# Optimization experiments

Measured on AMD Instinct MI355X. Metric: run time of the kernel, lower is better.

The kernel has to match this reference:

```python
import jax, jax.numpy as jnp
import numpy as np

B, H, W = 16, 16, 16
DIM = 768
NH = 8
HD = DIM // NH
NEXP = 8
TOPK = 2
DSTATE = 1
DTRANK = 4
KDIR = 4


def setup_inputs() -> dict:
    key = jax.random.key(0)
    ks = jax.random.split(key, 16)
    s = 1.0 / float(np.sqrt(DIM))
    inp = {
        'x': jax.random.normal(ks[0], (B, H, W, DIM)),
        'sa_in_w': jax.random.normal(ks[1], (3 * DIM, DIM)) * s,
        'sa_in_b': jnp.zeros((3 * DIM,)),
        'sa_out_w': jax.random.normal(ks[2], (DIM, DIM)) * s,
        'sa_out_b': jnp.zeros((DIM,)),
        'ca_in_w': jax.random.normal(ks[3], (2 * DIM, DIM)) * s,
        'ca_in_b': jnp.zeros((2 * DIM,)),
        'expert_queries': jax.random.normal(ks[4], (NEXP, DIM)) * s,
        'e_in_w': jax.random.normal(ks[5], (NEXP, 2 * DIM, DIM)) * s,
        'e_in_b': jnp.zeros((NEXP, 2 * DIM)),
        'e_conv_w': jax.random.normal(ks[6], (NEXP, DIM, 1, 3, 3)) / 3.0,
        'e_conv_b': jnp.zeros((NEXP, DIM)),
        'e_xproj_w': jax.random.normal(ks[7], (NEXP, KDIR, DTRANK + 2 * DSTATE, DIM)) * s,
        'e_dtproj_w': jax.random.normal(ks[8], (NEXP, KDIR, DIM, DTRANK)) * 0.1,
        'e_dtproj_b': jax.random.uniform(ks[9], (NEXP, KDIR, DIM), minval=-4.0, maxval=-2.0),
        'e_Alog': jax.random.uniform(ks[10], (NEXP, KDIR, DIM, DSTATE), minval=0.0, maxval=1.0),
        'e_D': jnp.ones((NEXP, KDIR, DIM)),
        'e_ln_scale': jnp.ones((NEXP, DIM)),
        'e_ln_bias': jnp.zeros((NEXP, DIM)),
    }
    return {k: v.astype(jnp.float32) for k, v in inp.items()}


def _selective_scan(xs, Wx, Wdt, bdt, Alog, D):
    # xs: [B, L, d]; Wx: [R+2N, d]; Wdt: [d, R]; Alog: [d, N]; D: [d]
    dbl = jnp.einsum('bld,ed->ble', xs, Wx)
    dt = jax.nn.softplus(jnp.einsum('blr,dr->bld', dbl[..., :DTRANK], Wdt) + bdt)
    Bm = dbl[..., DTRANK:DTRANK + DSTATE]
    Cm = dbl[..., DTRANK + DSTATE:]
    A = -jnp.exp(Alog)  # [d, N]

    def step(h, t):
        dt_t, B_t, C_t, x_t = t  # [b,d],[b,N],[b,N],[b,d]
        h = jnp.exp(dt_t[:, :, None] * A) * h + (dt_t * x_t)[:, :, None] * B_t[:, None, :]
        return h, jnp.einsum('bdn,bn->bd', h, C_t)

    b, L, d = xs.shape
    h0 = jnp.zeros((b, d, DSTATE), xs.dtype)
    tm = lambda a: jnp.moveaxis(a, 1, 0)
    _, ys = jax.lax.scan(step, h0, (tm(dt), tm(Bm), tm(Cm), tm(xs)))
    return jnp.moveaxis(ys, 0, 1) + D * xs


def _expert(in_w, in_b, conv_w, conv_b, xproj_w, dtp_w, dtp_b, Alog, D, ln_s, ln_b, x):
    b = x.shape[0]
    xz = jnp.einsum('bhwc,oc->bhwo', x, in_w) + in_b
    xc, z = jnp.split(xz, 2, axis=-1)
    xn = jax.lax.conv_general_dilated(jnp.transpose(xc, (0, 3, 1, 2)), conv_w,
                                      (1, 1), ((1, 1), (1, 1)), feature_group_count=DIM)
    xc = jax.nn.silu(jnp.transpose(xn + conv_b[None, :, None, None], (0, 2, 3, 1)))
    L = H * W
    xh = xc.reshape(b, L, DIM)                              # row-major 'h'
    xv = jnp.transpose(xc, (0, 2, 1, 3)).reshape(b, L, DIM)  # col-major 'v'
    seqs = jnp.stack([xh, xh[:, ::-1], xv, xv[:, ::-1]])     # [4, b, L, d]
    ys = jax.vmap(_selective_scan)(seqs, xproj_w, dtp_w, dtp_b, Alog, D)
    yv = ys[2] + ys[3][:, ::-1]
    yv = jnp.transpose(yv.reshape(b, W, H, DIM), (0, 2, 1, 3)).reshape(b, L, DIM)
    y = (ys[0] + ys[1][:, ::-1] + yv).reshape(b, H, W, DIM)
    mu = y.mean(-1, keepdims=True)
    var = ((y - mu) ** 2).mean(-1, keepdims=True)
    y = (y - mu) * jax.lax.rsqrt(var + 1e-5) * ln_s + ln_b   # out_norm (LayerNorm)
    y = y * jax.nn.silu(z)
    return y.mean((1, 2))  # AdaptiveAvgPool2d((1,1)) -> [b, DIM]


def _forward(x, sa_in_w, sa_in_b, sa_out_w, sa_out_b, ca_in_w, ca_in_b, expert_queries,
             e_in_w, e_in_b, e_conv_w, e_conv_b, e_xproj_w, e_dtproj_w, e_dtproj_b,
             e_Alog, e_D, e_ln_scale, e_ln_bias):
    b = x.shape[0]
    L = H * W
    scale = 1.0 / float(np.sqrt(HD))
    xs = x.reshape(b, L, DIM)
    # spatial self-attention (eval mode: dropout off)
    qkv = xs @ sa_in_w.T + sa_in_b
    q, k, v = [a.reshape(b, L, NH, HD) for a in jnp.split(qkv, 3, -1)]
    att = jax.nn.softmax(jnp.einsum('bqhd,bkhd->bhqk', q, k) * scale, -1)
    ctx = jnp.einsum('bhqk,bkhd->bqhd', att, v).reshape(b, L, DIM) @ sa_out_w.T + sa_out_b
    # expert cross-attention: only head-averaged attention weights are used
    q2 = (ctx @ ca_in_w[:DIM].T + ca_in_b[:DIM]).reshape(b, L, NH, HD)
    k2 = (expert_queries @ ca_in_w[DIM:].T + ca_in_b[DIM:]).reshape(NEXP, NH, HD)
    aw = jax.nn.softmax(jnp.einsum('blhd,ehd->bhle', q2, k2) * scale, -1).mean(1)  # [b,L,E]
    gate = jax.nn.softmax(aw.mean(1), -1)  # [b, E]
    tk_scores, tk_idx = jax.lax.top_k(gate, TOPK)
    wgt = jax.nn.softmax(tk_scores, -1)
    # dense expert compute (all experts on all samples), then gather top-k
    all_out = jax.vmap(_expert, in_axes=(0,) * 11 + (None,))(
        e_in_w, e_in_b, e_conv_w, e_conv_b, e_xproj_w, e_dtproj_w, e_dtproj_b,
        e_Alog, e_D, e_ln_scale, e_ln_bias, x)  # [E, b, DIM]
    per_b = jnp.transpose(all_out, (1, 0, 2))  # [b, E, DIM]
    sel = jnp.take_along_axis(per_b, tk_idx[:, :, None], axis=1)  # [b, K, DIM]
    return jnp.sum(wgt[:, :, None] * sel, axis=1)  # [b, DIM]


def reference(x, sa_in_w, sa_in_b, sa_out_w, sa_out_b, ca_in_w, ca_in_b, expert_queries,
              e_in_w, e_in_b, e_conv_w, e_conv_b, e_xproj_w, e_dtproj_w, e_dtproj_b,
              e_Alog, e_D, e_ln_scale, e_ln_bias):
    return _forward(x, sa_in_w, sa_in_b, sa_out_w, sa_out_b, ca_in_w, ca_in_b, expert_queries,
                    e_in_w, e_in_b, e_conv_w, e_conv_b, e_xproj_w, e_dtproj_w, e_dtproj_b,
                    e_Alog, e_D, e_ln_scale, e_ln_bias)
```

## Files before the change

### kernel.cpp

```cpp
#include <hip/hip_runtime.h>
#include <hip/hip_bf16.h>


#define LTOK 256
#define DIMC 768

typedef unsigned short ushortt;
typedef __attribute__((ext_vector_type(8))) short bf16x8;
typedef __attribute__((ext_vector_type(4))) float f32x4;

#define LOG2E 1.44269504f
#define LN2   0.69314718f

__device__ __forceinline__ float fexp2(float x) { return __builtin_amdgcn_exp2f(x); }
__device__ __forceinline__ float flog2(float x) { return __builtin_amdgcn_logf(x); }

__device__ __forceinline__ ushortt f2b(float f) {
  union { float f; unsigned u; } c; c.f = f;
  unsigned r = (c.u + 0x7FFFu + ((c.u >> 16) & 1u)) >> 16;
  return (ushortt)r;
}

__global__ __launch_bounds__(256) void mk_mcast4(
    const float* __restrict__ s0, ushortt* __restrict__ d0,
    const float* __restrict__ s1, ushortt* __restrict__ d1,
    const float* __restrict__ s2, ushortt* __restrict__ d2,
    const float* __restrict__ s3, ushortt* __restrict__ d3)
{
  long g = (long)blockIdx.x * 256 + threadIdx.x;
  const float* s; ushortt* dst; long o;
  if (g < 786432)       { s = s0; dst = d0; o = g; }
  else if (g < 1228800) { s = s1; dst = d1; o = g - 786432; }
  else if (g < 1376256) { s = s2; dst = d2; o = g - 1228800; }
  else                  { s = s3; dst = d3; o = g - 1376256; }
  o <<= 2;
  float4 v = *(const float4*)(s + o);
  ushort4 w;
  w.x = f2b(v.x); w.y = f2b(v.y); w.z = f2b(v.z); w.w = f2b(v.w);
  *(ushort4*)(dst + o) = w;
}

__global__ __launch_bounds__(256) void mk_cast(const float* __restrict__ in,
                                               ushortt* __restrict__ outp, long n)
{
  long i = ((long)blockIdx.x * 256 + threadIdx.x) * 4;
  if (i + 3 < n) {
    float4 v = *(const float4*)(in + i);
    ushort4 o;
    o.x = f2b(v.x); o.y = f2b(v.y); o.z = f2b(v.z); o.w = f2b(v.w);
    *(ushort4*)(outp + i) = o;
  }
}

__global__ __launch_bounds__(256) void mk_mfma(
    const ushortt* __restrict__ A, const ushortt* __restrict__ B,
    const float* __restrict__ bias, void* __restrict__ C,
    int K, int lda, int ldb, int ldc,
    long sA, long sB, long sC, long sBias,
    const int* __restrict__ pairExp, int tilesN,
    int outBf, int splitN, void* __restrict__ C2, int ldc2)
{
  int z = blockIdx.y;
  long aoff = 0, boff = 0, coff = 0, biasoff = 0;
  if (pairExp) {
    int e = pairExp[z];
    aoff = (long)(z >> 1) * sA; boff = (long)e * sB;
    coff = (long)z * sC; biasoff = (long)e * sBias;
  }
  int tile = blockIdx.x;
  int tm = tile / tilesN, tn = tile - tm * tilesN;
  long m0 = (long)tm << 7, n0 = (long)tn << 7;

  __shared__ ushortt As[128][40];
  __shared__ ushortt Bs[128][40];

  int tid = threadIdx.x;
  int lane = tid & 63, wvi = tid >> 6;
  int wr = wvi >> 1, wc = wvi & 1;
  int lm = lane & 15, lg = lane >> 4;

  f32x4 zero4 = {0.f, 0.f, 0.f, 0.f};
  f32x4 acc[4][4];
#pragma unroll
  for (int i = 0; i < 4; i++)
#pragma unroll
    for (int j = 0; j < 4; j++) acc[i][j] = zero4;

  const ushortt* Ab = A + aoff;
  const ushortt* Bb = B + boff;

  for (int k0 = 0; k0 < K; k0 += 32) {
#pragma unroll
    for (int h = 0; h < 2; h++) {
      int q = tid + h * 256;
      int row = q >> 2, ck = (q & 3) << 3;
      *(uint4*)&As[row][ck] = *(const uint4*)(Ab + (m0 + row) * lda + k0 + ck);
      *(uint4*)&Bs[row][ck] = *(const uint4*)(Bb + (n0 + row) * ldb + k0 + ck);
    }
    __syncthreads();
    bf16x8 af[4], bfr[4];
#pragma unroll
    for (int i = 0; i < 4; i++)
      af[i] = *(const bf16x8*)&As[wr * 64 + i * 16 + lm][lg << 3];
#pragma unroll
    for (int j = 0; j < 4; j++)
      bfr[j] = *(const bf16x8*)&Bs[wc * 64 + j * 16 + lm][lg << 3];
#pragma unroll
    for (int i = 0; i < 4; i++)
#pragma unroll
      for (int j = 0; j < 4; j++)
        acc[i][j] = __builtin_amdgcn_mfma_f32_16x16x32_bf16(af[i], bfr[j], acc[i][j], 0, 0, 0);
    __syncthreads();
  }

#pragma unroll
  for (int mt = 0; mt < 4; mt++) {
#pragma unroll
    for (int nt = 0; nt < 4; nt++) {
      long grow = m0 + wr * 64 + mt * 16 + lg * 4;
      long gcol = n0 + wc * 64 + nt * 16 + lm;
      float bv = bias ? bias[biasoff + gcol] : 0.f;
      void* Ct; long col; int ld;
      if ((int)gcol < splitN) { Ct = C; col = gcol; ld = ldc; }
      else { Ct = C2; col = gcol - splitN; ld = ldc2; }
#pragma unroll
      for (int r = 0; r < 4; r++) {
        float v = acc[mt][nt][r] + bv;
        long idx = coff + (grow + r) * ld + col;
        if (outBf) ((ushortt*)Ct)[idx] = f2b(v);
        else ((float*)Ct)[idx] = v;
      }
    }
  }
}

__global__ __launch_bounds__(256) void mk_gemm(
    const float* __restrict__ A, const float* __restrict__ B,
    const float* __restrict__ bias, void* __restrict__ C,
    int M, int N, int K, int lda, int ldb, int ldc,
    int zdiv,
    long sA1, long sA2, long sB1, long sB2, long sC1, long sC2,
    int bIsNT, int tilesN, int outBf)
{
  int z = blockIdx.y;
  int z1 = z / zdiv, z2 = z - z1 * zdiv;
  const float* Ab = A + (long)z1 * sA1 + (long)z2 * sA2;
  const float* Bb = B + (long)z1 * sB1 + (long)z2 * sB2;
  long coff = (long)z1 * sC1 + (long)z2 * sC2;

  int tile = blockIdx.x;
  int tm = tile / tilesN, tn = tile - tm * tilesN;
  int m0 = tm << 6, n0 = tn << 6;

  __shared__ float As[16][68];
  __shared__ float Bs[16][68];

  int tid = threadIdx.x;
  int tx = tid & 15, ty = tid >> 4;
  int lrow = tid >> 2;
  int lk = (tid & 3) << 2;
  int bkk = tid >> 4;
  int bnn = (tid & 15) << 2;

  float acc[4][4];
#pragma unroll
  for (int i = 0; i < 4; i++)
#pragma unroll
    for (int j = 0; j < 4; j++) acc[i][j] = 0.f;

  for (int k0 = 0; k0 < K; k0 += 16) {
    {
      int gm = m0 + lrow;
      float4 v = {0.f, 0.f, 0.f, 0.f};
      if (gm < M) v = *(const float4*)(Ab + (long)gm * lda + (k0 + lk));
      As[lk + 0][lrow] = v.x; As[lk + 1][lrow] = v.y;
      As[lk + 2][lrow] = v.z; As[lk + 3][lrow] = v.w;
    }
    if (bIsNT) {
      int gn = n0 + lrow;
      float4 v = {0.f, 0.f, 0.f, 0.f};
      if (gn < N) v = *(const float4*)(Bb + (long)gn * ldb + (k0 + lk));
      Bs[lk + 0][lrow] = v.x; Bs[lk + 1][lrow] = v.y;
      Bs[lk + 2][lrow] = v.z; Bs[lk + 3][lrow] = v.w;
    } else {
      int gn = n0 + bnn;
      float4 v = {0.f, 0.f, 0.f, 0.f};
      if (gn + 3 < N) {
        v = *(const float4*)(Bb + (long)(k0 + bkk) * ldb + gn);
      } else {
        float t0 = (gn + 0 < N) ? Bb[(long)(k0 + bkk) * ldb + gn + 0] : 0.f;
        float t1 = (gn + 1 < N) ? Bb[(long)(k0 + bkk) * ldb + gn + 1] : 0.f;
        float t2 = (gn + 2 < N) ? Bb[(long)(k0 + bkk) * ldb + gn + 2] : 0.f;
        float t3 = (gn + 3 < N) ? Bb[(long)(k0 + bkk) * ldb + gn + 3] : 0.f;
        v.x = t0; v.y = t1; v.z = t2; v.w = t3;
      }
      *(float4*)&Bs[bkk][bnn] = v;
    }
    __syncthreads();
#pragma unroll
    for (int kk = 0; kk < 16; kk++) {
      float4 a = *(const float4*)&As[kk][ty << 2];
      float4 b = *(const float4*)&Bs[kk][tx << 2];
      acc[0][0] += a.x * b.x; acc[0][1] += a.x * b.y; acc[0][2] += a.x * b.z; acc[0][3] += a.x * b.w;
      acc[1][0] += a.y * b.x; acc[1][1] += a.y * b.y; acc[1][2] += a.y * b.z; acc[1][3] += a.y * b.w;
      acc[2][0] += a.z * b.x; acc[2][1] += a.z * b.y; acc[2][2] += a.z * b.z; acc[2][3] += a.z * b.w;
      acc[3][0] += a.w * b.x; acc[3][1] += a.w * b.y; acc[3][2] += a.w * b.z; acc[3][3] += a.w * b.w;
    }
    __syncthreads();
  }

#pragma unroll
  for (int i = 0; i < 4; i++) {
    int gm = m0 + (ty << 2) + i;
    if (gm >= M) continue;
#pragma unroll
    for (int j = 0; j < 4; j++) {
      int gn = n0 + (tx << 2) + j;
      if (gn >= N) continue;
      float v = acc[i][j];
      if (bias) v += bias[gn];
      long idx = coff + (long)gm * ldc + gn;
      if (outBf) ((ushortt*)C)[idx] = f2b(v);
      else ((float*)C)[idx] = v;
    }
  }
}

__global__ __launch_bounds__(256) void mk_softmax(float* __restrict__ scores, float scale)
{
  int row = (blockIdx.x << 2) + (threadIdx.x >> 6);
  int lane = threadIdx.x & 63;
  float* p = scores + (long)row * 256 + (lane << 2);
  float4 v = *(const float4*)p;
  float m = fmaxf(fmaxf(v.x, v.y), fmaxf(v.z, v.w));
#pragma unroll
  for (int o = 32; o; o >>= 1) m = fmaxf(m, __shfl_xor(m, o, 64));
  float sl = scale * LOG2E;
  v.x = fexp2(sl * (v.x - m));
  v.y = fexp2(sl * (v.y - m));
  v.z = fexp2(sl * (v.z - m));
  v.w = fexp2(sl * (v.w - m));
  float s = v.x + v.y + v.z + v.w;
#pragma unroll
  for (int o = 32; o; o >>= 1) s += __shfl_xor(s, o, 64);
  float r = 1.f / s;
  v.x *= r; v.y *= r; v.z *= r; v.w *= r;
  *(float4*)p = v;
}

__global__ __launch_bounds__(256) void mk_gates(const float* __restrict__ q2,
                                                const float* __restrict__ k2,
                                                float* __restrict__ gacc)
{
  __shared__ float k2p[8 * 808];
  int b = blockIdx.x >> 4, q = blockIdx.x & 15;
  for (int i = threadIdx.x; i < 6144; i += 256) {
    int e = i / 768, rem = i - e * 768;
    int h = rem / 96, j = rem - h * 96;
    k2p[e * 808 + h * 100 + j] = k2[i];
  }
  __syncthreads();
  const float scale = 0.10206207261596577f;
  int wid = threadIdx.x >> 6, lane = threadIdx.x & 63;
  int h = lane >> 3, e = lane & 7;
  const float* kp = &k2p[e * 808 + h * 100];
  float accL = 0.f;
#pragma unroll
  for (int ti = 0; ti < 4; ti++) {
    int l = q * 16 + wid * 4 + ti;
    const float* qh = q2 + ((long)b * LTOK + l) * DIMC + h * 96;
    float sum = 0.f;
#pragma unroll
    for (int j = 0; j < 96; j += 4) {
      float4 qv = *(const float4*)(qh + j);
      float4 kv = *(const float4*)(kp + j);
      sum += qv.x * kv.x + qv.y * kv.y + qv.z * kv.z + qv.w * kv.w;
    }
    float s = sum * scale;
    float mx = s;
#pragma unroll
    for (int o = 1; o <= 4; o <<= 1) mx = fmaxf(mx, __shfl_xor(mx, o, 64));
    float ex = fexp2((s - mx) * LOG2E);
    float se = ex;
#pragma unroll
    for (int o = 1; o <= 4; o <<= 1) se += __shfl_xor(se, o, 64);
    accL += ex / se;
  }
#pragma unroll
  for (int o = 8; o <= 32; o <<= 1) accL += __shfl_xor(accL, o, 64);
  __shared__ float red[4][8];
  if (lane < 8) red[wid][lane] = accL;
  __syncthreads();
  if (threadIdx.x < 8) {
    float v = red[0][threadIdx.x] + red[1][threadIdx.x] +
              red[2][threadIdx.x] + red[3][threadIdx.x];
    atomicAdd(&gacc[b * 8 + threadIdx.x], v);
  }
}

__global__ __launch_bounds__(64) void mk_gatetop(const float* __restrict__ gacc,
                                                 int* __restrict__ pe,
                                                 float* __restrict__ pw)
{
  int b = threadIdx.x;
  if (b >= 16) return;
  float g[8];
  for (int e = 0; e < 8; e++) g[e] = gacc[b * 8 + e] * (1.f / (8.f * 256.f));
  float mx = g[0];
  for (int e = 1; e < 8; e++) mx = fmaxf(mx, g[e]);
  float se = 0.f;
  for (int e = 0; e < 8; e++) { g[e] = expf(g[e] - mx); se += g[e]; }
  for (int e = 0; e < 8; e++) g[e] /= se;
  int i0 = 0;
  for (int e = 1; e < 8; e++) if (g[e] > g[i0]) i0 = e;
  int i1 = (i0 == 0) ? 1 : 0;
  for (int e = 0; e < 8; e++) if (e != i0 && g[e] > g[i1]) i1 = e;
  float w0 = 1.f / (1.f + expf(g[i1] - g[i0]));
  pe[2 * b] = i0; pe[2 * b + 1] = i1;
  pw[2 * b] = w0; pw[2 * b + 1] = 1.f - w0;
}

__global__ __launch_bounds__(768) void mk_conv(const float* __restrict__ xzx,
                                               const float* __restrict__ cw,
                                               const float* __restrict__ cb,
                                               const int* __restrict__ pe,
                                               float* __restrict__ xc)
{
  int blk = blockIdx.x;
  int p = blk >> 8, t = blk & 255;
  int e = pe[p];
  int h = t >> 4, w = t & 15;
  int c = threadIdx.x;
  const float* wp = cw + ((long)e * DIMC + c) * 9;
  float acc = cb[e * DIMC + c];
#pragma unroll
  for (int dh = 0; dh < 3; dh++) {
    int hh = h + dh - 1;
    if (hh < 0 || hh > 15) continue;
#pragma unroll
    for (int dw = 0; dw < 3; dw++) {
      int ww = w + dw - 1;
      if (ww < 0 || ww > 15) continue;
      acc += xzx[((long)p * LTOK + hh * 16 + ww) * DIMC + c] * wp[dh * 3 + dw];
    }
  }
  xc[((long)p * LTOK + t) * DIMC + c] = acc / (1.f + fexp2(-acc * LOG2E));
}

__device__ __forceinline__ int tmap(int dir, int s) {
  if (dir == 0) return s;
  if (dir == 1) return 255 - s;
  if (dir == 2) return ((s & 15) << 4) | (s >> 4);
  int u = 255 - s;
  return ((u & 15) << 4) | (u >> 4);
}

__global__ __launch_bounds__(256) void mk_dbl(const float* __restrict__ xc,
                                              const float* __restrict__ xproj,
                                              const int* __restrict__ pe,
                                              float* __restrict__ dblm)
{
  int p = blockIdx.x >> 6;
  int tq = blockIdx.x & 63;
  int wid = threadIdx.x >> 6, lane = threadIdx.x & 63;
  int m = tq * 4 + wid;
  int e = pe[p];
  const float* xr = xc + ((long)p * LTOK + m) * DIMC;
  const float* wb = xproj + (long)e * 24 * DIMC;
  float4 xv[3];
#pragma unroll
  for (int j = 0; j < 3; j++) xv[j] = *(const float4*)(xr + j * 256 + lane * 4);
  float acc[24];
#pragma unroll
  for (int r = 0; r < 24; r++) {
    const float* wr = wb + r * DIMC;
    float s = 0.f;
#pragma unroll
    for (int j = 0; j < 3; j++) {
      float4 wv = *(const float4*)(wr + j * 256 + lane * 4);
      s += xv[j].x * wv.x + xv[j].y * wv.y + xv[j].z * wv.z + xv[j].w * wv.w;
    }
    acc[r] = s;
  }
#pragma unroll
  for (int r = 0; r < 24; r++)
#pragma unroll
    for (int o = 32; o; o >>= 1) acc[r] += __shfl_xor(acc[r], o, 64);
  if (lane == 0) {
    float* o = dblm + ((long)p * LTOK + m) * 24;
#pragma unroll
    for (int r = 0; r < 24; r++) o[r] = acc[r];
  }
}

__global__ __launch_bounds__(512) void mk_scan(const float* __restrict__ xc,
                                               const float* __restrict__ dblm,
                                               const float* __restrict__ dtw,
                                               const float* __restrict__ dtb,
                                               const float* __restrict__ Alog,
                                               const float* __restrict__ Dp,
                                               const int* __restrict__ pe,
                                               float* __restrict__ yac)
{
  __shared__ float dbS[256 * 24];
  __shared__ float yS[256 * 17];
  __shared__ float aS[32][16];
  __shared__ float hS[32][16];
  __shared__ float dsum[16];
  int blk = blockIdx.x;
  int p = blk / 48, cg = blk - p * 48;
  int c0 = cg << 4;
  int e = pe[p];
  int tid = threadIdx.x;
  {
    const float4* src = (const float4*)(dblm + (long)p * LTOK * 24);
    float4* dst = (float4*)dbS;
    for (int i = tid; i < 1536; i += 512) dst[i] = src[i];
  }
  for (int i = tid; i < 256 * 17; i += 512) yS[i] = 0.f;
  if (tid < 16) {
    float s = 0.f;
#pragma unroll
    for (int dd = 0; dd < 4; dd++) s += Dp[(long)(e * 4 + dd) * DIMC + c0 + tid];
    dsum[tid] = s;
  }
  __syncthreads();

  int c = tid & 15;
  int rr = tid >> 4;
  int seg = rr & 7;
  int dir = rr >> 3;
  int d = c0 + c;
  const float* xcp = xc + (long)p * LTOK * DIMC;
  long pb = (long)(e * 4 + dir) * DIMC + d;
  float4 wv = *(const float4*)(dtw + pb * 4);
  float bdt = dtb[pb];
  float Ad = -fexp2(Alog[pb] * LOG2E);
  int t0 = seg << 5;

  float h = 0.f, ap = 1.f;
  for (int tb = 0; tb < 32; tb += 8) {
    float xv[8]; int mm[8];
#pragma unroll
    for (int i = 0; i < 8; i++) {
      mm[i] = tmap(dir, t0 + tb + i);
      xv[i] = xcp[(long)mm[i] * DIMC + d];
    }
#pragma unroll
    for (int i = 0; i < 8; i++) {
      const float* db = &dbS[mm[i] * 24 + dir * 6];
      float xr = wv.x * db[0] + wv.y * db[1] + wv.z * db[2] + wv.w * db[3] + bdt;
      float te = fexp2(xr * LOG2E);
      float g = flog2(1.f + te);
      g = (xr > 60.f) ? xr * LOG2E : g;
      float de = fexp2(g * Ad);
      h = de * h + (g * LN2) * xv[i] * db[4];
      ap *= de;
    }
  }
  aS[rr][c] = ap;
  hS[rr][c] = h;
  __syncthreads();

  float hh = 0.f;
  for (int j = dir * 8; j < rr; j++)
    hh = aS[j][c] * hh + hS[j][c];

  for (int tb = 0; tb < 32; tb += 8) {
    float xv[8]; int mm[8];
#pragma unroll
    for (int i = 0; i < 8; i++) {
      mm[i] = tmap(dir, t0 + tb + i);
      xv[i] = xcp[(long)mm[i] * DIMC + d];
    }
#pragma unroll
    for (int i = 0; i < 8; i++) {
      const float* db = &dbS[mm[i] * 24 + dir * 6];
      float xr = wv.x * db[0] + wv.y * db[1] + wv.z * db[2] + wv.w * db[3] + bdt;
      float te = fexp2(xr * LOG2E);
      float g = flog2(1.f + te);
      g = (xr > 60.f) ? xr * LOG2E : g;
      float de = fexp2(g * Ad);
      hh = de * hh + (g * LN2) * xv[i] * db[4];
      atomicAdd(&yS[mm[i] * 17 + c], hh * db[5]);
    }
  }
  __syncthreads();

  float* yp = yac + (long)p * LTOK * DIMC + c0;
  for (int i = tid; i < 256 * 16; i += 512) {
    int t = i >> 4, cz = i & 15;
    yp[(long)t * DIMC + cz] = yS[t * 17 + cz] + xcp[(long)t * DIMC + c0 + cz] * dsum[cz];
  }
}

__global__ __launch_bounds__(768) void mk_lnfin(const float* __restrict__ yac,
                                                const float* __restrict__ xzz,
                                                const float* __restrict__ lns,
                                                const float* __restrict__ lnb,
                                                const int* __restrict__ pe,
                                                float* __restrict__ eo)
{
  int p = blockIdx.x;
  int e = pe[p];
  int tid = threadIdx.x;
  int wid = tid >> 6, lane = tid & 63;
  float ls[12], lb[12], acc[12];
#pragma unroll
  for (int i = 0; i < 12; i++) {
    int d = i * 64 + lane;
    ls[i] = lns[e * DIMC + d];
    lb[i] = lnb[e * DIMC + d];
    acc[i] = 0.f;
  }
  for (int t = wid; t < 256; t += 12) {
    const float* yr = yac + ((long)p * LTOK + t) * DIMC;
    const float* zr = xzz + ((long)p * LTOK + t) * DIMC;
    float v[12];
    float s = 0.f;
#pragma unroll
    for (int i = 0; i < 12; i++) { v[i] = yr[i * 64 + lane]; s += v[i]; }
#pragma unroll
    for (int o = 32; o; o >>= 1) s += __shfl_xor(s, o, 64);
    float mu = s * (1.f / 768.f);
    float sq = 0.f;
#pragma unroll
    for (int i = 0; i < 12; i++) { float dlt = v[i] - mu; sq += dlt * dlt; }
#pragma unroll
    for (int o = 32; o; o >>= 1) sq += __shfl_xor(sq, o, 64);
    float rs = rsqrtf(sq * (1.f / 768.f) + 1e-5f);
#pragma unroll
    for (int i = 0; i < 12; i++) {
      float y = (v[i] - mu) * rs * ls[i] + lb[i];
      float z = zr[i * 64 + lane];
      y *= z / (1.f + fexp2(-z * LOG2E));
      acc[i] += y;
    }
  }
  __shared__ float sacc[768];
  sacc[tid] = 0.f;
  __syncthreads();
#pragma unroll
  for (int i = 0; i < 12; i++) atomicAdd(&sacc[i * 64 + lane], acc[i]);
  __syncthreads();
  eo[(long)p * DIMC + tid] = sacc[tid] * (1.f / 256.f);
}

__global__ __launch_bounds__(768) void mk_out(const float* __restrict__ eo,
                                              const float* __restrict__ pw,
                                              float* __restrict__ out)
{
  int b = blockIdx.x, d = threadIdx.x;
  float v = pw[2 * b] * eo[(long)(2 * b) * DIMC + d] +
            pw[2 * b + 1] * eo[(long)(2 * b + 1) * DIMC + d];
  out[b * DIMC + d] = v;
}

extern "C" void kernel_launch(void* const* d_in, const int* in_sizes, int n_in,
                              void* d_out, int out_size, void* d_ws, size_t ws_size,
                              hipStream_t stream)
{
  const float* x        = (const float*)d_in[0];
  const float* sa_in_w  = (const float*)d_in[1];
  const float* sa_in_b  = (const float*)d_in[2];
  const float* sa_out_w = (const float*)d_in[3];
  const float* sa_out_b = (const float*)d_in[4];
  const float* ca_in_w  = (const float*)d_in[5];
  const float* ca_in_b  = (const float*)d_in[6];
  const float* eq       = (const float*)d_in[7];
  const float* e_in_w   = (const float*)d_in[8];
  const float* e_in_b   = (const float*)d_in[9];
  const float* e_conv_w = (const float*)d_in[10];
  const float* e_conv_b = (const float*)d_in[11];
  const float* e_xproj  = (const float*)d_in[12];
  const float* e_dtw    = (const float*)d_in[13];
  const float* e_dtb    = (const float*)d_in[14];
  const float* e_Alog   = (const float*)d_in[15];
  const float* e_D      = (const float*)d_in[16];
  const float* e_lns    = (const float*)d_in[17];
  const float* e_lnb    = (const float*)d_in[18];
  float* out = (float*)d_out;

  float* ws = (float*)d_ws;
  float*   qkv    = ws + 0;
  float*   scores = ws + 9437184;
  ushortt* ctxa_b = (ushortt*)(ws + 17825792);
  ushortt* xb     = (ushortt*)(ws + 20971520);
  ushortt* wqkv_b = (ushortt*)(ws + 22544384);
  ushortt* saow_b = (ushortt*)(ws + 23429120);
  ushortt* caw_b  = (ushortt*)(ws + 23724032);
  ushortt* ctx_b  = (ushortt*)(ws + 3145728);
  float*   q2     = ws + 4718592;
  float*   k2     = ws + 25165824;
  int*     pe     = (int*)(ws + 25171968);
  float*   pw     = ws + 25172000;
  float*   eo     = ws + 25172032;
  float*   dblm   = ws + 25196608;
  float*   gacc   = ws + 25393216;
  float*   xz_x   = ws + 0;
  float*   xz_z   = ws + 6291456;
  ushortt* ew_b   = (ushortt*)(ws + 12582912);
  float*   xc     = ws + 12582912;
  float*   yac    = ws + 18874368;

  const float scale = 0.10206207261596577f;

  mk_mcast4<<<5952, 256, 0, stream>>>(x, xb, sa_in_w, wqkv_b, sa_out_w, saow_b,
                                      ca_in_w, caw_b);
  mk_mfma<<<dim3(32 * 18, 1), 256, 0, stream>>>(xb, wqkv_b, sa_in_b, qkv,
      768, 768, 768, 2304, 0, 0, 0, 0, nullptr, 18, 0, 1 << 30, nullptr, 0);
  mk_gemm<<<dim3(16, 128), 256, 0, stream>>>(qkv, qkv + 768, nullptr, scores,
      256, 256, 96, 2304, 2304, 256, 8, 589824, 96, 589824, 96, 524288, 65536, 1, 4, 0);
  mk_softmax<<<8192, 256, 0, stream>>>(scores, scale);
  mk_gemm<<<dim3(8, 128), 256, 0, stream>>>(scores, qkv + 1536, nullptr, ctxa_b,
      256, 96, 256, 256, 2304, 768, 8, 524288, 65536, 589824, 96, 196608, 96, 0, 2, 1);
  mk_cast<<<9216, 256, 0, stream>>>(e_in_w, ew_b, 9437184);
  mk_mfma<<<dim3(32 * 6, 1), 256, 0, stream>>>(ctxa_b, saow_b, sa_out_b, ctx_b,
      768, 768, 768, 768, 0, 0, 0, 0, nullptr, 6, 1, 1 << 30, nullptr, 0);
  mk_mfma<<<dim3(32 * 6, 1), 256, 0, stream>>>(ctx_b, caw_b, ca_in_b, q2,
      768, 768, 768, 768, 0, 0, 0, 0, nullptr, 6, 0, 1 << 30, nullptr, 0);
  mk_gemm<<<dim3(12, 1), 256, 0, stream>>>(eq, ca_in_w + 589824, ca_in_b + 768, k2,
      8, 768, 768, 768, 768, 768, 1, 0, 0, 0, 0, 0, 0, 1, 12, 0);
  (void)hipMemsetAsync(gacc, 0, 128 * sizeof(float), stream);
  mk_gates<<<256, 256, 0, stream>>>(q2, k2, gacc);
  mk_gatetop<<<1, 64, 0, stream>>>(gacc, pe, pw);
  mk_mfma<<<dim3(2 * 12, 32), 256, 0, stream>>>(xb, ew_b, e_in_b, xz_x,
      768, 768, 768, 768, 196608, 1179648, 196608, 1536, pe, 12, 0, 768, xz_z, 768);
  mk_conv<<<32 * 256, 768, 0, stream>>>(xz_x, e_conv_w, e_conv_b, pe, xc);
  mk_dbl<<<2048, 256, 0, stream>>>(xc, e_xproj, pe, dblm);
  mk_scan<<<1536, 512, 0, stream>>>(xc, dblm, e_dtw, e_dtb, e_Alog, e_D, pe, yac);
  mk_lnfin<<<32, 768, 0, stream>>>(yac, xz_z, e_lns, e_lnb, pe, eo);
  mk_out<<<16, 768, 0, stream>>>(eo, pw, out);

  (void)in_sizes; (void)n_in; (void)out_size; (void)ws_size;
}
```

Measured before the change: 708.4 us.

## Move self-attention matmuls to bf16 MFMA and split LayerNorm-pool across blocks

The QKV projection now writes Q/K as bf16 and V transposed per head, so QK^T and attn·V run on the bf16 MFMA kernel instead of the fp32 SIMT GEMM. Softmax now emits bf16 probabilities for that purpose. The LN-pool kernel is split into 512 blocks of 256 threads that atomically accumulate into a zeroed buffer, and the 1/256 mean is moved into mk_out. This trades the precision of attention scores and probabilities for tensor-core throughput. It also adds a memset and global atomics, which make the accumulation order nondeterministic.

```diff
diff --git a/kernel.cpp b/kernel.cpp
--- a/kernel.cpp
+++ b/kernel.cpp
@@ -56,16 +56,22 @@
     const ushortt* __restrict__ A, const ushortt* __restrict__ B,
     const float* __restrict__ bias, void* __restrict__ C,
     int K, int lda, int ldb, int ldc,
-    long sA, long sB, long sC, long sBias,
+    int zdiv, long sA1, long sA2, long sB1, long sB2, long sC1, long sC2,
+    long sBias,
     const int* __restrict__ pairExp, int tilesN,
-    int outBf, int splitN, void* __restrict__ C2, int ldc2)
+    int outBf, int splitN, void* __restrict__ C2, int ldc2, int outBf2, int c2vt)
 {
   int z = blockIdx.y;
-  long aoff = 0, boff = 0, coff = 0, biasoff = 0;
+  long aoff, boff, coff, biasoff = 0;
   if (pairExp) {
     int e = pairExp[z];
-    aoff = (long)(z >> 1) * sA; boff = (long)e * sB;
-    coff = (long)z * sC; biasoff = (long)e * sBias;
+    aoff = (long)(z >> 1) * sA1; boff = (long)e * sB1;
+    coff = (long)z * sC1; biasoff = (long)e * sBias;
+  } else {
+    int z1 = z / zdiv, z2 = z - z1 * zdiv;
+    aoff = (long)z1 * sA1 + (long)z2 * sA2;
+    boff = (long)z1 * sB1 + (long)z2 * sB2;
+    coff = (long)z1 * sC1 + (long)z2 * sC2;
   }
   int tile = blockIdx.x;
   int tm = tile / tilesN, tn = tile - tm * tilesN;
@@ -120,15 +126,34 @@
       long grow = m0 + wr * 64 + mt * 16 + lg * 4;
       long gcol = n0 + wc * 64 + nt * 16 + lm;
       float bv = bias ? bias[biasoff + gcol] : 0.f;
-      void* Ct; long col; int ld;
-      if ((int)gcol < splitN) { Ct = C; col = gcol; ld = ldc; }
-      else { Ct = C2; col = gcol - splitN; ld = ldc2; }
-#pragma unroll
-      for (int r = 0; r < 4; r++) {
-        float v = acc[mt][nt][r] + bv;
-        long idx = coff + (grow + r) * ld + col;
-        if (outBf) ((ushortt*)Ct)[idx] = f2b(v);
-        else ((float*)Ct)[idx] = v;
+      if ((int)gcol < splitN) {
+#pragma unroll
+        for (int r = 0; r < 4; r++) {
+          float v = acc[mt][nt][r] + bv;
+          long idx = coff + (grow + r) * ldc + gcol;
+          if (outBf) ((ushortt*)C)[idx] = f2b(v);
+          else ((float*)C)[idx] = v;
+        }
+      } else if (c2vt) {
+        int cc = (int)gcol - splitN;
+        int hh = cc / 96, jj = cc - hh * 96;
+#pragma unroll
+        for (int r = 0; r < 4; r++) {
+          float v = acc[mt][nt][r] + bv;
+          long gr = grow + r;
+          long b = gr >> 8, t = gr & 255;
+          long idx = (((b * 8 + hh) * 128 + jj) << 8) + t;
+          ((ushortt*)C2)[idx] = f2b(v);
+        }
+      } else {
+        long col = gcol - splitN;
+#pragma unroll
+        for (int r = 0; r < 4; r++) {
+          float v = acc[mt][nt][r] + bv;
+          long idx = coff + (grow + r) * ldc2 + col;
+          if (outBf2) ((ushortt*)C2)[idx] = f2b(v);
+          else ((float*)C2)[idx] = v;
+        }
       }
     }
   }
@@ -136,18 +161,9 @@
 
 __global__ __launch_bounds__(256) void mk_gemm(
     const float* __restrict__ A, const float* __restrict__ B,
-    const float* __restrict__ bias, void* __restrict__ C,
-    int M, int N, int K, int lda, int ldb, int ldc,
-    int zdiv,
-    long sA1, long sA2, long sB1, long sB2, long sC1, long sC2,
-    int bIsNT, int tilesN, int outBf)
-{
-  int z = blockIdx.y;
-  int z1 = z / zdiv, z2 = z - z1 * zdiv;
-  const float* Ab = A + (long)z1 * sA1 + (long)z2 * sA2;
-  const float* Bb = B + (long)z1 * sB1 + (long)z2 * sB2;
-  long coff = (long)z1 * sC1 + (long)z2 * sC2;
-
+    const float* __restrict__ bias, float* __restrict__ C,
+    int M, int N, int K, int lda, int ldb, int ldc, int tilesN)
+{
   int tile = blockIdx.x;
   int tm = tile / tilesN, tn = tile - tm * tilesN;
   int m0 = tm << 6, n0 = tn << 6;
@@ -159,8 +175,6 @@
   int tx = tid & 15, ty = tid >> 4;
   int lrow = tid >> 2;
   int lk = (tid & 3) << 2;
-  int bkk = tid >> 4;
-  int bnn = (tid & 15) << 2;
 
   float acc[4][4];
 #pragma unroll
@@ -172,29 +186,16 @@
     {
       int gm = m0 + lrow;
       float4 v = {0.f, 0.f, 0.f, 0.f};
-      if (gm < M) v = *(const float4*)(Ab + (long)gm * lda + (k0 + lk));
+      if (gm < M) v = *(const float4*)(A + (long)gm * lda + (k0 + lk));
       As[lk + 0][lrow] = v.x; As[lk + 1][lrow] = v.y;
       As[lk + 2][lrow] = v.z; As[lk + 3][lrow] = v.w;
     }
-    if (bIsNT) {
+    {
       int gn = n0 + lrow;
       float4 v = {0.f, 0.f, 0.f, 0.f};
-      if (gn < N) v = *(const float4*)(Bb + (long)gn * ldb + (k0 + lk));
+      if (gn < N) v = *(const float4*)(B + (long)gn * ldb + (k0 + lk));
       Bs[lk + 0][lrow] = v.x; Bs[lk + 1][lrow] = v.y;
       Bs[lk + 2][lrow] = v.z; Bs[lk + 3][lrow] = v.w;
-    } else {
-      int gn = n0 + bnn;
-      float4 v = {0.f, 0.f, 0.f, 0.f};
-      if (gn + 3 < N) {
-        v = *(const float4*)(Bb + (long)(k0 + bkk) * ldb + gn);
-      } else {
-        float t0 = (gn + 0 < N) ? Bb[(long)(k0 + bkk) * ldb + gn + 0] : 0.f;
-        float t1 = (gn + 1 < N) ? Bb[(long)(k0 + bkk) * ldb + gn + 1] : 0.f;
-        float t2 = (gn + 2 < N) ? Bb[(long)(k0 + bkk) * ldb + gn + 2] : 0.f;
-        float t3 = (gn + 3 < N) ? Bb[(long)(k0 + bkk) * ldb + gn + 3] : 0.f;
-        v.x = t0; v.y = t1; v.z = t2; v.w = t3;
-      }
-      *(float4*)&Bs[bkk][bnn] = v;
     }
     __syncthreads();
 #pragma unroll
@@ -219,18 +220,17 @@
       if (gn >= N) continue;
       float v = acc[i][j];
       if (bias) v += bias[gn];
-      long idx = coff + (long)gm * ldc + gn;
-      if (outBf) ((ushortt*)C)[idx] = f2b(v);
-      else ((float*)C)[idx] = v;
-    }
-  }
-}
-
-__global__ __launch_bounds__(256) void mk_softmax(float* __restrict__ scores, float scale)
+      C[(long)gm * ldc + gn] = v;
+    }
+  }
+}
+
+__global__ __launch_bounds__(256) void mk_softmax(const float* __restrict__ scores,
+                                                  ushortt* __restrict__ att, float scale)
 {
   int row = (blockIdx.x << 2) + (threadIdx.x >> 6);
   int lane = threadIdx.x & 63;
-  float* p = scores + (long)row * 256 + (lane << 2);
+  const float* p = scores + (long)row * 256 + (lane << 2);
   float4 v = *(const float4*)p;
   float m = fmaxf(fmaxf(v.x, v.y), fmaxf(v.z, v.w));
 #pragma unroll
@@ -244,8 +244,9 @@
 #pragma unroll
   for (int o = 32; o; o >>= 1) s += __shfl_xor(s, o, 64);
   float r = 1.f / s;
-  v.x *= r; v.y *= r; v.z *= r; v.w *= r;
-  *(float4*)p = v;
+  ushort4 o4;
+  o4.x = f2b(v.x * r); o4.y = f2b(v.y * r); o4.z = f2b(v.z * r); o4.w = f2b(v.w * r);
+  *(ushort4*)(att + (long)row * 256 + (lane << 2)) = o4;
 }
 
 __global__ __launch_bounds__(256) void mk_gates(const float* __restrict__ q2,
@@ -494,14 +495,15 @@
   }
 }
 
-__global__ __launch_bounds__(768) void mk_lnfin(const float* __restrict__ yac,
+__global__ __launch_bounds__(256) void mk_lnfin(const float* __restrict__ yac,
                                                 const float* __restrict__ xzz,
                                                 const float* __restrict__ lns,
                                                 const float* __restrict__ lnb,
                                                 const int* __restrict__ pe,
                                                 float* __restrict__ eo)
 {
-  int p = blockIdx.x;
+  int blk = blockIdx.x;
+  int p = blk >> 4, ts = blk & 15;
   int e = pe[p];
   int tid = threadIdx.x;
   int wid = tid >> 6, lane = tid & 63;
@@ -513,7 +515,9 @@
     lb[i] = lnb[e * DIMC + d];
     acc[i] = 0.f;
   }
-  for (int t = wid; t < 256; t += 12) {
+#pragma unroll
+  for (int tt = 0; tt < 4; tt++) {
+    int t = ts * 16 + wid * 4 + tt;
     const float* yr = yac + ((long)p * LTOK + t) * DIMC;
     const float* zr = xzz + ((long)p * LTOK + t) * DIMC;
     float v[12];
@@ -538,12 +542,12 @@
     }
   }
   __shared__ float sacc[768];
-  sacc[tid] = 0.f;
+  for (int j = tid; j < 768; j += 256) sacc[j] = 0.f;
   __syncthreads();
 #pragma unroll
   for (int i = 0; i < 12; i++) atomicAdd(&sacc[i * 64 + lane], acc[i]);
   __syncthreads();
-  eo[(long)p * DIMC + tid] = sacc[tid] * (1.f / 256.f);
+  for (int j = tid; j < 768; j += 256) atomicAdd(&eo[(long)p * DIMC + j], sacc[j]);
 }
 
 __global__ __launch_bounds__(768) void mk_out(const float* __restrict__ eo,
@@ -553,7 +557,7 @@
   int b = blockIdx.x, d = threadIdx.x;
   float v = pw[2 * b] * eo[(long)(2 * b) * DIMC + d] +
             pw[2 * b + 1] * eo[(long)(2 * b + 1) * DIMC + d];
-  out[b * DIMC + d] = v;
+  out[b * DIMC + d] = v * (1.f / 256.f);
 }
 
 extern "C" void kernel_launch(void* const* d_in, const int* in_sizes, int n_in,
@@ -582,15 +586,18 @@
   float* out = (float*)d_out;
 
   float* ws = (float*)d_ws;
-  float*   qkv    = ws + 0;
-  float*   scores = ws + 9437184;
-  ushortt* ctxa_b = (ushortt*)(ws + 17825792);
+  ushortt* qk_b   = (ushortt*)(ws + 0);
+  float*   scores = ws + 6291456;
+  ushortt* dump_b = (ushortt*)(ws + 6291456);
+  ushortt* ctxa_b = (ushortt*)(ws + 7864320);
+  ushortt* att_b  = (ushortt*)(ws + 14680064);
+  ushortt* vt_b   = (ushortt*)(ws + 18874368);
   ushortt* xb     = (ushortt*)(ws + 20971520);
   ushortt* wqkv_b = (ushortt*)(ws + 22544384);
   ushortt* saow_b = (ushortt*)(ws + 23429120);
   ushortt* caw_b  = (ushortt*)(ws + 23724032);
-  ushortt* ctx_b  = (ushortt*)(ws + 3145728);
-  float*   q2     = ws + 4718592;
+  ushortt* ctx_b  = (ushortt*)(ws + 0);
+  float*   q2     = ws + 1572864;
   float*   k2     = ws + 25165824;
   int*     pe     = (int*)(ws + 25171968);
   float*   pw     = ws + 25172000;
@@ -607,29 +614,36 @@
 
   mk_mcast4<<<5952, 256, 0, stream>>>(x, xb, sa_in_w, wqkv_b, sa_out_w, saow_b,
                                       ca_in_w, caw_b);
-  mk_mfma<<<dim3(32 * 18, 1), 256, 0, stream>>>(xb, wqkv_b, sa_in_b, qkv,
-      768, 768, 768, 2304, 0, 0, 0, 0, nullptr, 18, 0, 1 << 30, nullptr, 0);
-  mk_gemm<<<dim3(16, 128), 256, 0, stream>>>(qkv, qkv + 768, nullptr, scores,
-      256, 256, 96, 2304, 2304, 256, 8, 589824, 96, 589824, 96, 524288, 65536, 1, 4, 0);
-  mk_softmax<<<8192, 256, 0, stream>>>(scores, scale);
-  mk_gemm<<<dim3(8, 128), 256, 0, stream>>>(scores, qkv + 1536, nullptr, ctxa_b,
-      256, 96, 256, 256, 2304, 768, 8, 524288, 65536, 589824, 96, 196608, 96, 0, 2, 1);
+  mk_mfma<<<dim3(576, 1), 256, 0, stream>>>(xb, wqkv_b, sa_in_b, qk_b,
+      768, 768, 768, 1536, 1, 0, 0, 0, 0, 0, 0, 0, nullptr, 18,
+      1, 1536, vt_b, 0, 1, 1);
+  mk_mfma<<<dim3(4, 128), 256, 0, stream>>>(qk_b, qk_b + 768, nullptr, scores,
+      96, 1536, 1536, 256, 8, 393216, 96, 393216, 96, 524288, 65536, 0, nullptr, 2,
+      0, 1 << 30, nullptr, 0, 0, 0);
+  mk_softmax<<<8192, 256, 0, stream>>>(scores, att_b, scale);
+  mk_mfma<<<dim3(2, 128), 256, 0, stream>>>(att_b, vt_b, nullptr, ctxa_b,
+      256, 256, 256, 768, 8, 524288, 65536, 262144, 32768, 196608, 96, 0, nullptr, 1,
+      1, 96, dump_b, 32, 1, 0);
   mk_cast<<<9216, 256, 0, stream>>>(e_in_w, ew_b, 9437184);
-  mk_mfma<<<dim3(32 * 6, 1), 256, 0, stream>>>(ctxa_b, saow_b, sa_out_b, ctx_b,
-      768, 768, 768, 768, 0, 0, 0, 0, nullptr, 6, 1, 1 << 30, nullptr, 0);
-  mk_mfma<<<dim3(32 * 6, 1), 256, 0, stream>>>(ctx_b, caw_b, ca_in_b, q2,
-      768, 768, 768, 768, 0, 0, 0, 0, nullptr, 6, 0, 1 << 30, nullptr, 0);
+  mk_mfma<<<dim3(192, 1), 256, 0, stream>>>(ctxa_b, saow_b, sa_out_b, ctx_b,
+      768, 768, 768, 768, 1, 0, 0, 0, 0, 0, 0, 0, nullptr, 6,
+      1, 1 << 30, nullptr, 0, 0, 0);
+  mk_mfma<<<dim3(192, 1), 256, 0, stream>>>(ctx_b, caw_b, ca_in_b, q2,
+      768, 768, 768, 768, 1, 0, 0, 0, 0, 0, 0, 0, nullptr, 6,
+      0, 1 << 30, nullptr, 0, 0, 0);
   mk_gemm<<<dim3(12, 1), 256, 0, stream>>>(eq, ca_in_w + 589824, ca_in_b + 768, k2,
-      8, 768, 768, 768, 768, 768, 1, 0, 0, 0, 0, 0, 0, 1, 12, 0);
+      8, 768, 768, 768, 768, 768, 12);
   (void)hipMemsetAsync(gacc, 0, 128 * sizeof(float), stream);
+  (void)hipMemsetAsync(eo, 0, 24576 * sizeof(float), stream);
   mk_gates<<<256, 256, 0, stream>>>(q2, k2, gacc);
   mk_gatetop<<<1, 64, 0, stream>>>(gacc, pe, pw);
-  mk_mfma<<<dim3(2 * 12, 32), 256, 0, stream>>>(xb, ew_b, e_in_b, xz_x,
-      768, 768, 768, 768, 196608, 1179648, 196608, 1536, pe, 12, 0, 768, xz_z, 768);
+  mk_mfma<<<dim3(24, 32), 256, 0, stream>>>(xb, ew_b, e_in_b, xz_x,
+      768, 768, 768, 768, 1, 196608, 0, 1179648, 0, 196608, 0, 1536, pe, 12,
+      0, 768, xz_z, 768, 0, 0);
   mk_conv<<<32 * 256, 768, 0, stream>>>(xz_x, e_conv_w, e_conv_b, pe, xc);
   mk_dbl<<<2048, 256, 0, stream>>>(xc, e_xproj, pe, dblm);
   mk_scan<<<1536, 512, 0, stream>>>(xc, dblm, e_dtw, e_dtb, e_Alog, e_D, pe, yac);
-  mk_lnfin<<<32, 768, 0, stream>>>(yac, xz_z, e_lns, e_lnb, pe, eo);
+  mk_lnfin<<<512, 256, 0, stream>>>(yac, xz_z, e_lns, e_lnb, pe, eo);
   mk_out<<<16, 768, 0, stream>>>(eo, pw, out);
 
   (void)in_sizes; (void)n_in; (void)out_size; (void)ws_size;
```

New measurement: 641.8 us. 9.4% less time.
